# Performance work log

Hardware: AMD Instinct MI355X
Metric: run time of the kernel (lower is better)

The kernel has to match this reference:

```python
import jax, jax.numpy as jnp
import numpy as np
import math

MAX_L = 8                       # spherical-harmonic max degree
R = 0.95                        # poincare disk radius
ENERGY_THR = 0.9999
GOLDEN = 0.618033988749
LM = [(l, m) for l in range(MAX_L + 1) for m in range(-l, l + 1)]  # 81 pairs


def _assoc_legendre(x, l, m):
    # m >= 0, standard upward recurrence; x is a vector
    if l == 0 and m == 0:
        return jnp.ones_like(x)
    pmm = jnp.ones_like(x)
    if m > 0:
        somx2 = jnp.sqrt(1.0 - x * x)
        fact = 1.0
        for _ in range(m):
            pmm = pmm * (-fact * somx2)
            fact += 2.0
    if l == m:
        return pmm
    pmmp1 = x * (2 * m + 1) * pmm
    if l == m + 1:
        return pmmp1
    pll, plp1 = pmm, pmmp1
    for ll in range(m + 2, l + 1):
        pnew = ((2 * ll - 1) * x * plp1 - (ll + m - 1) * pll) / (ll - m)
        pll, plp1 = plp1, pnew
    return plp1


def _harmonic(cos_t, phi, l, m):
    P = _assoc_legendre(cos_t, l, abs(m))
    norm = math.sqrt((2 * l + 1) * math.factorial(l - abs(m))
                     / math.factorial(l + abs(m)) / (4.0 * math.pi))
    ang = jnp.cos(m * phi) if m >= 0 else jnp.sin(abs(m) * phi)
    return norm * P * ang


def _sphere_coords(zr, zi):
    # hyperbolic radius -> polar angle on sphere; phi = complex argument
    r = jnp.sqrt(zr * zr + zi * zi)
    phi = jnp.arctan2(zi, zr)
    cos_t = jnp.cos(2.0 * jnp.arctanh(jnp.minimum(r, 0.99)) * math.pi / (2.0 * MAX_L))
    return cos_t, phi


def _forward_transform(w):
    flat = w.reshape(-1)
    if flat.shape[0] % 2 == 1:
        flat = jnp.concatenate([flat, jnp.zeros((1,), flat.dtype)])
    re, im = flat[0::2], flat[1::2]
    mag = jnp.sqrt(re * re + im * im)
    scale = jnp.max(mag)
    safe = jnp.where(scale > 0, scale, 1.0)
    a, b = re / safe, im / safe
    # complex tanh(a+ib) = (sinh 2a + i sin 2b) / (cosh 2a + cos 2b)
    den = jnp.cosh(2 * a) + jnp.cos(2 * b)
    pr = jnp.where(scale > 0, jnp.sinh(2 * a) / den * R, re)
    pi_ = jnp.where(scale > 0, jnp.sin(2 * b) / den * R, im)
    cos_t, phi = _sphere_coords(pr, pi_)
    coeffs = jnp.stack([jnp.mean(_harmonic(cos_t, phi, l, m)) for l, m in LM])
    return coeffs, scale, re.shape[0]


def _compress(c):
    # adaptive top-energy masking (decompress restores zeros -> masking is exact)
    n = c.shape[0]
    mag = jnp.abs(c)
    order = jnp.argsort(-mag)
    e = jnp.cumsum(mag[order] ** 2)
    tot = e[-1]
    kc = jnp.where(tot > 0,
                   jnp.sum(e / jnp.maximum(tot, 1e-30) <= ENERGY_THR) + 1,
                   n)
    kc = jnp.maximum(kc, n // 2)
    ranks = jnp.zeros((n,), jnp.int32).at[order].set(jnp.arange(n, dtype=jnp.int32))
    return jnp.where(ranks < kc, c, 0.0)


def _inverse_transform(c, scale, num_points, shape):
    i = jnp.arange(num_points, dtype=jnp.float32)
    r = jnp.minimum((i + 0.5) / num_points * R, 0.95)
    theta = jnp.mod(2.0 * math.pi * i * GOLDEN, 1.0)
    zr, zi = r * jnp.cos(theta), r * jnp.sin(theta)
    cos_t, phi = _sphere_coords(zr, zi)
    cm = jnp.where(jnp.abs(c) > 1e-10, c, 0.0)
    recon = jnp.zeros((num_points,), jnp.float32)
    for idx, (l, m) in enumerate(LM):
        recon = recon + cm[idx] * _harmonic(cos_t, phi, l, m)
    real = jnp.where(scale > 0, recon * scale, recon)
    # interleave (real, imag=0) as in torch stack([re, im], 1).flatten()
    flat = jnp.stack([real, jnp.zeros_like(real)], axis=1).reshape(-1)
    total = int(np.prod(shape))
    if flat.shape[0] > total:
        flat = flat[:total]
    elif flat.shape[0] < total:
        flat = jnp.concatenate([flat, jnp.zeros((total - flat.shape[0],), flat.dtype)])
    return flat.reshape(shape)


def setup_inputs() -> dict:
    key = jax.random.key(0)
    ks = jax.random.split(key, 5)
    return {
        "x": jax.random.normal(ks[0], (8, 1024, 768), jnp.float32),
        "w_fc": jax.random.normal(ks[1], (2, 3072, 768), jnp.float32) * 0.02,
        "w_proj": jax.random.normal(ks[2], (2, 768, 3072), jnp.float32) * 0.02,
        "b_fc": jax.random.normal(ks[3], (2, 3072), jnp.float32) * 0.02,
        "b_proj": jax.random.normal(ks[4], (2, 768), jnp.float32) * 0.02,
    }


def reference(x, w_fc, w_proj, b_fc, b_proj):
    L = w_fc.shape[0]
    imp = jax.nn.softmax(jnp.arange(L, dtype=jnp.float32) * 0.5)
    fused_fc = jnp.einsum('l,lij->ij', imp, w_fc)
    fused_proj = jnp.einsum('l,lij->ij', imp, w_proj)
    bias_fc = jnp.einsum('l,li->i', imp, b_fc)
    bias_proj = jnp.einsum('l,li->i', imp, b_proj)

    c_fc, s_fc, n_fc = _forward_transform(fused_fc)
    W_fc = _inverse_transform(_compress(c_fc), s_fc, n_fc, fused_fc.shape)
    c_pr, s_pr, n_pr = _forward_transform(fused_proj)
    W_proj = _inverse_transform(_compress(c_pr), s_pr, n_pr, fused_proj.shape)

    h = jax.nn.gelu(jnp.einsum('bsd,fd->bsf', x, W_fc) + bias_fc, approximate=False)
    return jnp.einsum('bsf,df->bsd', h, W_proj) + bias_proj
```

## Files before the change

### kernel.cpp

```cpp
#include <hip/hip_runtime.h>

#define MAXL 8
#define NC 81
#define NPAIR 1179648
#define TOTW  2359296
#define PI_F 3.14159265358979323846f
#define CO_BLOCKS 256

typedef __attribute__((ext_vector_type(8))) __bf16 bf16x8;
typedef __attribute__((ext_vector_type(4))) float f32x4;
typedef __attribute__((address_space(3))) void lds_void;
typedef const __attribute__((address_space(1))) void glb_void;

constexpr double cfact(int n){ double r=1.0; for(int i=2;i<=n;++i) r*=(double)i; return r; }
constexpr double csqrtd(double x){
  double r = (x > 1.0) ? x : 1.0;
  for (int i=0;i<200;++i) r = 0.5*(r + x/r);
  return r;
}
struct Norms { float v[NC]; };
constexpr Norms make_norms(){
  Norms t{};
  for (int l=0;l<=MAXL;++l)
    for (int m=-l;m<=l;++m){
      int am = m<0?-m:m;
      double nn = csqrtd((double)(2*l+1)*cfact(l-am)/cfact(l+am)/(4.0*3.14159265358979323846));
      t.v[l*l+l+m] = (float)nn;
    }
  return t;
}
__constant__ Norms g_norm = make_norms();

__device__ __forceinline__ float fast_atanh(float x){
  return 0.5f * __logf((1.0f + x) * __builtin_amdgcn_rcpf(1.0f - x));
}

__global__ void k_init(unsigned* scaleBits, double* gacc){
  int t = threadIdx.x;
  if (t < 2) scaleBits[t] = 0u;
  if (t < 2*NC) gacc[t] = 0.0;
}

__global__ __launch_bounds__(256) void k_max(const float* __restrict__ wfc,
    const float* __restrict__ wpr, unsigned* __restrict__ scaleBits,
    float imp0, float imp1){
  const int mat = blockIdx.y;
  const float2* w0 = (const float2*)(mat ? wpr : wfc);
  const float2* w1 = w0 + (TOTW/2);
  float vmax = 0.0f;
  for (int i = blockIdx.x*blockDim.x + threadIdx.x; i < NPAIR; i += gridDim.x*blockDim.x){
    float2 a = w0[i], b = w1[i];
    float re = fmaf(imp0, a.x, imp1*b.x);
    float im = fmaf(imp0, a.y, imp1*b.y);
    vmax = fmaxf(vmax, sqrtf(re*re + im*im));
  }
  for (int off=32; off; off>>=1) vmax = fmaxf(vmax, __shfl_down(vmax, off));
  __shared__ float red[4];
  int lane = threadIdx.x & 63, wv = threadIdx.x >> 6;
  if (lane == 0) red[wv] = vmax;
  __syncthreads();
  if (threadIdx.x == 0){
    float m = fmaxf(fmaxf(red[0], red[1]), fmaxf(red[2], red[3]));
    atomicMax(scaleBits + mat, __float_as_uint(m));
  }
}

__global__ __launch_bounds__(256,2) void k_coeff(const float* __restrict__ wfc,
                                                 const float* __restrict__ wpr,
                                                 const unsigned* __restrict__ scaleBits,
                                                 double* __restrict__ gacc){
  const int mat = blockIdx.y;
  const float2* w0 = (const float2*)(mat ? wpr : wfc);
  const float2* w1 = w0 + (TOTW/2);
  const float scale = __uint_as_float(scaleBits[mat]);
  const bool has = scale > 0.0f;
  const float inv_safe = 1.0f / (has ? scale : 1.0f);
  const float imp0 = (float)0.37754066879814546;
  const float imp1 = (float)0.62245933120185454;

  float acc[NC];
  #pragma unroll
  for (int v=0; v<NC; ++v) acc[v] = 0.0f;

  auto map1 = [&](int idx, float& X, float& c1, float& s1, float& st){
    float2 av = w0[idx], bv = w1[idx];
    float re = fmaf(imp0, av.x, imp1*bv.x);
    float im = fmaf(imp0, av.y, imp1*bv.y);
    float pr, pi_;
    if (has){
      float a = re*inv_safe, b = im*inv_safe;
      float e  = __expf(2.0f*a);
      float ie = __builtin_amdgcn_rcpf(e);
      float ch = 0.5f*(e + ie), sh = 0.5f*(e - ie);
      float s2b, c2b; __sincosf(2.0f*b, &s2b, &c2b);
      float inv_den = __builtin_amdgcn_rcpf(ch + c2b);
      pr  = sh*inv_den*0.95f;
      pi_ = s2b*inv_den*0.95f;
    } else { pr = re; pi_ = im; }
    float r2 = pr*pr + pi_*pi_;
    float inv_r = (r2 > 0.0f) ? __builtin_amdgcn_rsqf(r2) : 0.0f;
    c1 = (r2 > 0.0f) ? pr*inv_r : 1.0f;
    s1 = pi_*inv_r;
    float rr_ = r2*inv_r;
    float arg = fast_atanh(fminf(rr_, 0.99f)) * (PI_F/8.0f);
    __sincosf(arg, &st, &X);
  };

  const int T = CO_BLOCKS*256;
  for (int i = blockIdx.x*blockDim.x + threadIdx.x; i < NPAIR/2; i += T){
    float X0,c10,s10,st0, X1,c11,s11,st1;
    map1(i,           X0, c10, s10, st0);
    map1(i + NPAIR/2, X1, c11, s11, st1);

    float cm0=1.0f, sm0=0.0f, pm0=1.0f;
    float cm1=1.0f, sm1=0.0f, pm1=1.0f;
    float fact=1.0f;
    #pragma unroll
    for (int m=0; m<=MAXL; ++m){
      if (m > 0){
        float t0 = cm0*c10 - sm0*s10; sm0 = sm0*c10 + cm0*s10; cm0 = t0;
        float t1 = cm1*c11 - sm1*s11; sm1 = sm1*c11 + cm1*s11; cm1 = t1;
        pm0 = pm0 * (-fact*st0);
        pm1 = pm1 * (-fact*st1);
        fact += 2.0f;
      }
      float a1 = pm0, b1 = pm1;
      acc[m*m + 2*m] += a1*cm0 + b1*cm1;
      if (m > 0) acc[m*m] += a1*sm0 + b1*sm1;
      if (m < MAXL){
        float a0 = a1, b0 = b1;
        a1 = X0*(float)(2*m+1)*a0;
        b1 = X1*(float)(2*m+1)*b0;
        acc[(m+1)*(m+1) + (m+1) + m] += a1*cm0 + b1*cm1;
        if (m > 0) acc[(m+1)*(m+1) + 1] += a1*sm0 + b1*sm1;
        #pragma unroll
        for (int l=m+2; l<=MAXL; ++l){
          float an = ((float)(2*l-1)*X0*a1 - (float)(l+m-1)*a0) * (1.0f/(float)(l-m));
          a0 = a1; a1 = an;
          float bn = ((float)(2*l-1)*X1*b1 - (float)(l+m-1)*b0) * (1.0f/(float)(l-m));
          b0 = b1; b1 = bn;
          acc[l*l + l + m] += a1*cm0 + b1*cm1;
          if (m > 0) acc[l*l + l - m] += a1*sm0 + b1*sm1;
        }
      }
    }
  }

  __shared__ float redf[4][NC];
  int lane = threadIdx.x & 63, wv = threadIdx.x >> 6;
  #pragma unroll
  for (int v=0; v<NC; ++v){
    float d = acc[v];
    for (int off=32; off; off>>=1) d += __shfl_down(d, off);
    if (lane == 0) redf[wv][v] = d;
  }
  __syncthreads();
  for (int v = threadIdx.x; v < NC; v += blockDim.x){
    double s = (double)redf[0][v] + (double)redf[1][v] + (double)redf[2][v] + (double)redf[3][v];
    unsafeAtomicAdd(gacc + mat*NC + v, s);
  }
}

__global__ __launch_bounds__(128) void k_compress(const double* __restrict__ gacc,
                                                  float* __restrict__ cfin){
  const int mat = blockIdx.x;
  const int v = threadIdx.x;
  __shared__ float mg[NC];
  __shared__ float smg2[NC];
  __shared__ int cnt_sh;

  float c = 0.0f, m = -1.0f;
  if (v < NC){
    double m_ = (double)g_norm.v[v] * gacc[mat*NC + v] / (double)NPAIR;
    c = (float)m_;
    m = fabsf(c);
    mg[v] = m;
  }
  if (v == 0) cnt_sh = 0;
  __syncthreads();

  int rank = 0;
  if (v < NC){
    #pragma unroll 1
    for (int u = 0; u < NC; ++u){
      float mu = mg[u];
      rank += (mu > m) || (mu == m && u < v);
    }
    smg2[rank] = m*m;
  }
  __syncthreads();

  float e_mine = 0.0f, tot = 0.0f;
  if (v < NC){
    float run = 0.0f;
    #pragma unroll 1
    for (int u = 0; u < NC; ++u){
      run += smg2[u];
      if (u == rank) e_mine = run;
    }
    tot = run;
    float den = fmaxf(tot, 1e-30f);
    if (tot > 0.0f && (e_mine / den <= 0.9999f)) atomicAdd(&cnt_sh, 1);
  }
  __syncthreads();

  if (v < NC){
    int kc = (tot > 0.0f) ? (cnt_sh + 1) : NC;
    if (kc < NC/2) kc = NC/2;
    float cv = (rank < kc) ? c : 0.0f;
    if (fabsf(cv) <= 1e-10f) cv = 0.0f;
    cfin[mat*NC + v] = cv;
  }
}

__global__ __launch_bounds__(256) void k_inverse(const float* __restrict__ cfin,
    const unsigned* __restrict__ scaleBits, __bf16* __restrict__ B1, __bf16* __restrict__ B2){
  __shared__ float cA[NC], cB[NC], sc[2];
  if (threadIdx.x < NC){ cA[threadIdx.x] = cfin[threadIdx.x]; cB[threadIdx.x] = cfin[NC + threadIdx.x]; }
  if (threadIdx.x < 2) sc[threadIdx.x] = __uint_as_float(scaleBits[threadIdx.x]);
  __syncthreads();
  int j = blockIdx.x*blockDim.x + threadIdx.x;
  if (j >= NPAIR) return;

  float jf = (float)j;
  float r = fminf((jf + 0.5f) / 1179648.0f * 0.95f, 0.95f);
  float theta = fmodf((6.28318530717958647692f * jf) * 0.618033988749f, 1.0f);
  float phi = theta;
  float X, sint;
  {
    float arg = fast_atanh(fminf(r, 0.99f)) * (PI_F/8.0f);
    __sincosf(arg, &sint, &X);
  }
  float s1, c1; __sincosf(phi, &s1, &c1);

  float ra = 0.0f, rb = 0.0f;
  float cm = 1.0f, sm = 0.0f, pmm = 1.0f, fact = 1.0f;

  auto emit = [&](int l, int m, float P){
    int ip = l*l + l + m;
    float y = g_norm.v[ip] * P;
    float yc = y*cm;
    ra += cA[ip]*yc; rb += cB[ip]*yc;
    if (m > 0){
      int in_ = l*l + l - m;
      float ys = y*sm;
      ra += cA[in_]*ys; rb += cB[in_]*ys;
    }
  };

  #pragma unroll
  for (int m=0; m<=MAXL; ++m){
    if (m > 0){
      float t = cm*c1 - sm*s1;
      sm = sm*c1 + cm*s1;
      cm = t;
      pmm = pmm * (-fact*sint);
      fact += 2.0f;
    }
    float p0 = pmm;
    emit(m, m, p0);
    if (m < MAXL){
      float p1 = X*(float)(2*m+1)*p0;
      emit(m+1, m, p1);
      #pragma unroll
      for (int l=m+2; l<=MAXL; ++l){
        float pn = ((float)(2*l-1)*X*p1 - (float)(l+m-1)*p0) * (1.0f/(float)(l-m));
        p0 = p1; p1 = pn;
        emit(l, m, p1);
      }
    }
  }

  float sA = sc[0], sB = sc[1];
  B2[j] = (__bf16)((sB > 0.0f) ? rb*sB : rb);
  int q = j / 768, rem = j - q*768;
  if (rem < 384)
    B1[q*384 + rem] = (__bf16)((sA > 0.0f) ? ra*sA : ra);
}

__global__ void k_gather(const float* __restrict__ x, __bf16* __restrict__ A1){
  int t = blockIdx.x*blockDim.x + threadIdx.x;
  if (t < 8192*384){
    float2 v = ((const float2*)x)[t];
    A1[t] = (__bf16)v.x;
  }
}

template<int ACT, int OUTBF, int MI, int NJ>
__global__ __launch_bounds__(256) void k_gemm_mfma(
    const __bf16* __restrict__ A, const __bf16* __restrict__ B,
    const float* __restrict__ bias, int bmul, int blen,
    float imp0, float imp1,
    __bf16* __restrict__ Hout, float* __restrict__ Fout,
    int N, int K)
{
  constexpr int BM = 2*MI*16, BN = 2*NJ*16;
  constexpr int ACH = BM/16, NCH = (BM+BN)/16;
  __shared__ __bf16 As[BM*32];
  __shared__ __bf16 Bs[BN*32];
  const int tid  = threadIdx.x;
  const int wave = tid >> 6, lane = tid & 63;
  const int wr = wave >> 1, wc = wave & 1;
  const int rr = lane & 15, kq = lane >> 4;
  const int bm = blockIdx.y * BM, bn = blockIdx.x * BN;

  const int grow = lane >> 2;
  const int gcol = (lane & 3) * 8;
  const __bf16* Abase = A + (size_t)bm * K;
  const __bf16* Bbase = B + (size_t)bn * K;

  f32x4 acc[MI][NJ] = {};

  for (int k0 = 0; k0 < K; k0 += 32) {
    #pragma unroll
    for (int is = 0; is < NCH/4; ++is) {
      const int c = is * 4 + wave;
      if (c < ACH) {
        const __bf16* ga = Abase + (size_t)(c*16 + grow) * K + (k0 + gcol);
        __builtin_amdgcn_global_load_lds((glb_void*)ga, (lds_void*)(As + c*512), 16, 0, 0);
      } else {
        const int cb = c - ACH;
        const __bf16* gb = Bbase + (size_t)(cb*16 + grow) * K + (k0 + gcol);
        __builtin_amdgcn_global_load_lds((glb_void*)gb, (lds_void*)(Bs + cb*512), 16, 0, 0);
      }
    }
    __syncthreads();

    bf16x8 af[MI], bfr[NJ];
    #pragma unroll
    for (int i=0;i<MI;++i) af[i]  = *(const bf16x8*)&As[(wr*MI*16 + i*16 + rr)*32 + kq*8];
    #pragma unroll
    for (int j=0;j<NJ;++j) bfr[j] = *(const bf16x8*)&Bs[(wc*NJ*16 + j*16 + rr)*32 + kq*8];
    #pragma unroll
    for (int i=0;i<MI;++i)
      #pragma unroll
      for (int j=0;j<NJ;++j)
        acc[i][j] = __builtin_amdgcn_mfma_f32_16x16x32_bf16(af[i], bfr[j], acc[i][j], 0, 0, 0);
    __syncthreads();
  }

  #pragma unroll
  for (int j=0;j<NJ;++j){
    const int col = bn + wc*NJ*16 + j*16 + rr;
    const float bb = imp0*bias[bmul*col] + imp1*bias[blen + bmul*col];
    #pragma unroll
    for (int i=0;i<MI;++i){
      const int row0 = bm + wr*MI*16 + i*16 + kq*4;
      #pragma unroll
      for (int t=0;t<4;++t){
        float v = acc[i][j][t] + bb;
        if (ACT) v = 0.5f*v*(1.0f + erff(v*0.70710678118654752440f));
        if (OUTBF) Hout[(size_t)(row0+t)*N + col] = (__bf16)v;
        else       Fout[(size_t)(row0+t)*N + col] = v;
      }
    }
  }
}

extern "C" void kernel_launch(void* const* d_in, const int* in_sizes, int n_in,
                              void* d_out, int out_size, void* d_ws, size_t ws_size,
                              hipStream_t stream){
  const float* x   = (const float*)d_in[0];
  const float* wfc = (const float*)d_in[1];
  const float* wpr = (const float*)d_in[2];
  const float* bfc = (const float*)d_in[3];
  const float* bpr = (const float*)d_in[4];
  float* out = (float*)d_out;

  char* ws = (char*)d_ws;
  size_t off = 0;
  auto alloc = [&](size_t bytes){ void* p = ws + off; off = (off + bytes + 255) & ~(size_t)255; return p; };

  unsigned* scaleBits= (unsigned*)alloc(8);
  double* gacc       = (double*)  alloc(2*NC*sizeof(double));
  float* cfin        = (float*)   alloc(2*NC*sizeof(float));
  __bf16* B1         = (__bf16*)  alloc((size_t)1536*384*sizeof(__bf16));
  __bf16* B2         = (__bf16*)  alloc((size_t)768*1536*sizeof(__bf16));
  __bf16* A1         = (__bf16*)  alloc((size_t)8192*384*sizeof(__bf16));
  __bf16* H          = (__bf16*)  alloc((size_t)8192*1536*sizeof(__bf16));

  const float imp0 = (float)0.37754066879814546;
  const float imp1 = (float)0.62245933120185454;

  k_init<<<1,256,0,stream>>>(scaleBits, gacc);
  k_max<<<dim3(128,2),256,0,stream>>>(wfc, wpr, scaleBits, imp0, imp1);
  k_coeff<<<dim3(CO_BLOCKS,2),256,0,stream>>>(wfc, wpr, scaleBits, gacc);
  k_compress<<<2,128,0,stream>>>(gacc, cfin);
  k_inverse<<<4608,256,0,stream>>>(cfin, scaleBits, B1, B2);
  k_gather<<<12288,256,0,stream>>>(x, A1);
  k_gemm_mfma<1,1,4,4><<<dim3(12,64),256,0,stream>>>(A1, B1, bfc, 2, 3072, imp0, imp1, H, nullptr, 1536, 384);
  k_gemm_mfma<0,0,4,2><<<dim3(12,64),256,0,stream>>>(H, B2, bpr, 1, 768, imp0, imp1, nullptr, out, 768, 1536);
}
```

Before: 177.6 us.

## Double-buffer GEMM LDS tiles with XOR swizzle and widen max-reduction grid

```diff
diff --git a/kernel.cpp b/kernel.cpp
--- a/kernel.cpp
+++ b/kernel.cpp
@@ -296,46 +296,64 @@
 {
   constexpr int BM = 2*MI*16, BN = 2*NJ*16;
   constexpr int ACH = BM/16, NCH = (BM+BN)/16;
-  __shared__ __bf16 As[BM*32];
-  __shared__ __bf16 Bs[BN*32];
+  static_assert(NCH % 4 == 0, "chunks must split across 4 waves");
+  __shared__ __bf16 As[2][BM*32];
+  __shared__ __bf16 Bs[2][BN*32];
   const int tid  = threadIdx.x;
   const int wave = tid >> 6, lane = tid & 63;
   const int wr = wave >> 1, wc = wave & 1;
   const int rr = lane & 15, kq = lane >> 4;
+  const int sx = rr & 3;
   const int bm = blockIdx.y * BM, bn = blockIdx.x * BN;
 
-  const int grow = lane >> 2;
-  const int gcol = (lane & 3) * 8;
+  const int lrow  = lane >> 2;
+  const int lslot = lane & 3;
+  const int sslot = lslot ^ (lrow & 3);
   const __bf16* Abase = A + (size_t)bm * K;
   const __bf16* Bbase = B + (size_t)bn * K;
 
   f32x4 acc[MI][NJ] = {};
 
-  for (int k0 = 0; k0 < K; k0 += 32) {
+  auto stage = [&](int buf, int k0){
     #pragma unroll
     for (int is = 0; is < NCH/4; ++is) {
       const int c = is * 4 + wave;
       if (c < ACH) {
-        const __bf16* ga = Abase + (size_t)(c*16 + grow) * K + (k0 + gcol);
-        __builtin_amdgcn_global_load_lds((glb_void*)ga, (lds_void*)(As + c*512), 16, 0, 0);
+        const __bf16* ga = Abase + (size_t)(c*16 + lrow) * K + (k0 + sslot*8);
+        __builtin_amdgcn_global_load_lds((glb_void*)ga, (lds_void*)(&As[buf][c*512]), 16, 0, 0);
       } else {
         const int cb = c - ACH;
-        const __bf16* gb = Bbase + (size_t)(cb*16 + grow) * K + (k0 + gcol);
-        __builtin_amdgcn_global_load_lds((glb_void*)gb, (lds_void*)(Bs + cb*512), 16, 0, 0);
+        const __bf16* gb = Bbase + (size_t)(cb*16 + lrow) * K + (k0 + sslot*8);
+        __builtin_amdgcn_global_load_lds((glb_void*)gb, (lds_void*)(&Bs[buf][cb*512]), 16, 0, 0);
       }
     }
-    __syncthreads();
+  };
+
+  const int nt = K/32;
+  stage(0, 0);
+  __syncthreads();
+
+  for (int t = 0; t < nt; ++t) {
+    const int cur = t & 1;
+    if (t + 1 < nt) stage(cur ^ 1, (t+1)*32);
 
     bf16x8 af[MI], bfr[NJ];
     #pragma unroll
-    for (int i=0;i<MI;++i) af[i]  = *(const bf16x8*)&As[(wr*MI*16 + i*16 + rr)*32 + kq*8];
-    #pragma unroll
-    for (int j=0;j<NJ;++j) bfr[j] = *(const bf16x8*)&Bs[(wc*NJ*16 + j*16 + rr)*32 + kq*8];
+    for (int i=0;i<MI;++i){
+      const int row = wr*MI*16 + i*16 + rr;
+      af[i]  = *(const bf16x8*)&As[cur][row*32 + ((kq ^ sx) << 3)];
+    }
+    #pragma unroll
+    for (int j=0;j<NJ;++j){
+      const int row = wc*NJ*16 + j*16 + rr;
+      bfr[j] = *(const bf16x8*)&Bs[cur][row*32 + ((kq ^ sx) << 3)];
+    }
     #pragma unroll
     for (int i=0;i<MI;++i)
       #pragma unroll
       for (int j=0;j<NJ;++j)
         acc[i][j] = __builtin_amdgcn_mfma_f32_16x16x32_bf16(af[i], bfr[j], acc[i][j], 0, 0, 0);
+
     __syncthreads();
   }
 
@@ -383,7 +401,7 @@
   const float imp1 = (float)0.62245933120185454;
 
   k_init<<<1,256,0,stream>>>(scaleBits, gacc);
-  k_max<<<dim3(128,2),256,0,stream>>>(wfc, wpr, scaleBits, imp0, imp1);
+  k_max<<<dim3(256,2),256,0,stream>>>(wfc, wpr, scaleBits, imp0, imp1);
   k_coeff<<<dim3(CO_BLOCKS,2),256,0,stream>>>(wfc, wpr, scaleBits, gacc);
   k_compress<<<2,128,0,stream>>>(gacc, cfin);
   k_inverse<<<4608,256,0,stream>>>(cfin, scaleBits, B1, B2);
```

Result: faster. 172.8 us (-2.7%).
